# Kernel optimization log

Hardware: AMD Instinct MI355X
Metric: run time of the kernel (lower is better)

Reference implementation:

```python
import jax, jax.numpy as jnp
import numpy as np

N = 30000      # nodes
E = 300000     # edges (before self-loops)
F_NODE = 32; F_EDGE = 16
HID = 64       # hidden_channels
H = 4; C = 64  # heads, per-head channels (GATConv out_channels = HID)
NEG_SLOPE_ATT = 0.2   # GATConv negative_slope
NEG_SLOPE_ACT = 0.01  # F.leaky_relu default
LN_EPS = 1e-5


def setup_inputs() -> dict:
    key = jax.random.key(0)
    ks = jax.random.split(key, 32)
    def w(k, shape, fan_in):
        return jax.random.normal(k, shape, jnp.float32) * (1.0 / np.sqrt(fan_in))
    inp = {
        "x": jax.random.normal(ks[0], (N, F_NODE), jnp.float32),
        "edge_index": jax.random.randint(ks[1], (2, E), 0, N),
        "edge_attr": jax.random.normal(ks[2], (E, F_EDGE), jnp.float32),
        "wn": w(ks[3], (F_NODE, HID), F_NODE), "bn": jnp.zeros((HID,), jnp.float32),
        "we": w(ks[4], (F_EDGE, HID), F_EDGE), "be": jnp.zeros((HID,), jnp.float32),
    }
    for i, off in ((1, 5), (2, 13)):
        inp[f"lin{i}"] = w(ks[off], (HID, H * C), HID)        # GATConv.lin
        inp[f"line{i}"] = w(ks[off + 1], (HID, H * C), HID)    # GATConv.lin_edge
        inp[f"as{i}"] = w(ks[off + 2], (H, C), C)              # att_src
        inp[f"ad{i}"] = w(ks[off + 3], (H, C), C)              # att_dst
        inp[f"ae{i}"] = w(ks[off + 4], (H, C), C)              # att_edge
        inp[f"b{i}"] = jnp.zeros((C,), jnp.float32)            # GATConv bias (concat=False -> C)
        inp[f"g{i}"] = jnp.ones((HID,), jnp.float32)           # LayerNorm weight
        inp[f"bt{i}"] = jnp.zeros((HID,), jnp.float32)         # LayerNorm bias
    return inp


def layernorm(x, g, b):
    mu = x.mean(-1, keepdims=True)
    v = ((x - mu) ** 2).mean(-1, keepdims=True)
    return (x - mu) / jnp.sqrt(v + LN_EPS) * g + b


def gat_layer(x, src, dst, e_attr, lin_w, lin_e_w, att_src, att_dst, att_edge, bias, n):
    # x: [n, HID]; e_attr: [E2, HID]; edge lists already include self-loops
    E2 = src.shape[0]
    h = (x @ lin_w).reshape(n, H, C)          # [n,H,C]
    e = (e_attr @ lin_e_w).reshape(E2, H, C)  # [E2,H,C]
    a_src = (h * att_src[None]).sum(-1)       # [n,H]
    a_dst = (h * att_dst[None]).sum(-1)       # [n,H]
    a_edge = (e * att_edge[None]).sum(-1)     # [E2,H]
    a = jax.nn.leaky_relu(a_src[src] + a_dst[dst] + a_edge, NEG_SLOPE_ATT)
    # scatter-softmax over destination neighborhoods (every node has a self-loop)
    m = jax.ops.segment_max(a, dst, num_segments=n)
    ex = jnp.exp(a - m[dst])
    den = jax.ops.segment_sum(ex, dst, num_segments=n)
    alpha = ex / den[dst]                     # [E2,H]
    out = jax.ops.segment_sum(h[src] * alpha[..., None], dst, num_segments=n)  # [n,H,C]
    return out.mean(axis=1) + bias, alpha     # concat=False: average heads


def reference(x, edge_index, edge_attr, wn, bn, we, be,
              lin1, line1, as1, ad1, ae1, b1, g1, bt1,
              lin2, line2, as2, ad2, ae2, b2, g2, bt2):
    n = x.shape[0]
    x = jax.nn.relu(x @ wn + bn)
    ea = jax.nn.relu(edge_attr @ we + be)
    src, dst = edge_index[0], edge_index[1]
    # PyG add_self_loops(fill_value='mean'): self-loop edge_attr = mean of incoming edge_attr
    ones = jnp.ones((src.shape[0],), ea.dtype)
    deg = jax.ops.segment_sum(ones, dst, num_segments=n)
    mean_ea = jax.ops.segment_sum(ea, dst, num_segments=n) / jnp.maximum(deg, 1.0)[:, None]
    loop = jnp.arange(n, dtype=src.dtype)
    src_f = jnp.concatenate([src, loop])
    dst_f = jnp.concatenate([dst, loop])
    ea_f = jnp.concatenate([ea, mean_ea], axis=0)
    h1, alpha1 = gat_layer(x, src_f, dst_f, ea_f, lin1, line1, as1, ad1, ae1, b1, n)
    h1 = layernorm(jax.nn.leaky_relu(h1, NEG_SLOPE_ACT), g1, bt1)
    # dropout is identity in eval mode
    h2, alpha2 = gat_layer(h1, src_f, dst_f, ea_f, lin2, line2, as2, ad2, ae2, b2, n)
    h2 = layernorm(jax.nn.leaky_relu(h2, NEG_SLOPE_ACT), g2, bt2)
    return h2, alpha1, alpha2
```

## Files before the change

kernel.cpp:

```cpp
#include <hip/hip_runtime.h>

#define FN 32
#define FE 16
#define HID 64
#define HEADS 4
#define CHC 64

typedef float f32x4 __attribute__((ext_vector_type(4)));

__device__ __forceinline__ float bf2f(unsigned short u) {
  unsigned int x = ((unsigned int)u) << 16;
  return __builtin_bit_cast(float, x);
}
__device__ __forceinline__ unsigned short f2bf(float f) {
  unsigned int x = __builtin_bit_cast(unsigned int, f);
  unsigned int r = (x + 0x7fff + ((x >> 16) & 1)) >> 16;
  return (unsigned short)r;
}
__device__ __forceinline__ unsigned int pack2bf(float a, float b) {
  return (unsigned int)f2bf(a) | ((unsigned int)f2bf(b) << 16);
}

__global__ __launch_bounds__(256) void k_vecs(
    const float* __restrict__ lin1, const float* __restrict__ line1,
    const float* __restrict__ as1, const float* __restrict__ ad1,
    const float* __restrict__ ae1,
    const float* __restrict__ lin2, const float* __restrict__ line2,
    const float* __restrict__ as2, const float* __restrict__ ad2,
    const float* __restrict__ ae2,
    float* __restrict__ vS, float* __restrict__ vD, float* __restrict__ vE)
{
  int bi = blockIdx.x;
  int l = bi / 3, kind = bi % 3;
  const float* lin = (kind == 2) ? (l ? line2 : line1) : (l ? lin2 : lin1);
  const float* att = (kind == 0) ? (l ? as2 : as1)
                   : (kind == 1) ? (l ? ad2 : ad1) : (l ? ae2 : ae1);
  float* out = ((kind == 0) ? vS : (kind == 1) ? vD : vE) + l * 256;
  int t = threadIdx.x;
  int c = t >> 2, hd = t & 3;
  float acc = 0.f;
  for (int cc = 0; cc < CHC; cc++)
    acc += lin[c * (HEADS * CHC) + hd * CHC + cc] * att[hd * CHC + cc];
  out[c * 4 + hd] = acc;
}

__global__ __launch_bounds__(256) void k_deg(const int* __restrict__ dst,
                                             int* __restrict__ deg, int E)
{
  int e = blockIdx.x * 256 + threadIdx.x;
  if (e < E) atomicAdd(&deg[dst[e]], 1);
}

__global__ __launch_bounds__(1024) void k_scan1(const int* __restrict__ deg,
    int* __restrict__ rowptr, int* __restrict__ bsum, int n)
{
  __shared__ int wsum[16];
  int t = threadIdx.x, wv = t >> 6, lane = t & 63;
  int i = blockIdx.x * 1024 + t;
  int val = (i < n) ? deg[i] : 0;
  int sc = val;
  #pragma unroll
  for (int off = 1; off < 64; off <<= 1) {
    int u = __shfl_up(sc, off);
    if (lane >= off) sc += u;
  }
  if (lane == 63) wsum[wv] = sc;
  __syncthreads();
  int woff = 0;
  #pragma unroll
  for (int k = 0; k < 16; k++) woff += (k < wv) ? wsum[k] : 0;
  if (i < n) rowptr[i] = woff + sc - val;
  if (t == 0) {
    int tot = 0;
    #pragma unroll
    for (int k = 0; k < 16; k++) tot += wsum[k];
    bsum[blockIdx.x] = tot;
  }
}

__global__ __launch_bounds__(1024) void k_scan23(const int* __restrict__ bsum,
    int* __restrict__ rowptr, int nb, int n)
{
  int b = blockIdx.x;
  int t = threadIdx.x;
  int off = 0;
  for (int j = 0; j < b; j++) off += bsum[j];
  int i = b * 1024 + t;
  if (i < n) rowptr[i] += off;
  if (b == 0 && t == 0) {
    int tot = 0;
    for (int j = 0; j < nb; j++) tot += bsum[j];
    rowptr[n] = tot;
  }
}

__global__ __launch_bounds__(256) void k_fill(const int* __restrict__ src,
    const int* __restrict__ dst, const int* __restrict__ rowptr,
    int* __restrict__ cnt, int* __restrict__ eid, int* __restrict__ srcs,
    int* __restrict__ perm, int E)
{
  int e = blockIdx.x * 256 + threadIdx.x;
  if (e < E) {
    int d = dst[e];
    int pos = rowptr[d] + atomicAdd(&cnt[d], 1);
    eid[pos] = e;
    srcs[pos] = src[e];
    perm[e] = pos;
  }
}

__global__ __launch_bounds__(256) void k_aeg_e(const float* __restrict__ eattr,
    const float* __restrict__ we, const float* __restrict__ be,
    const float* __restrict__ vE, const int* __restrict__ perm,
    float* __restrict__ aeg1, float* __restrict__ aeg2, int E)
{
  __shared__ float4 we_t4[HID][4];
  __shared__ float4 vE_s[2][HID];
  __shared__ float  be_s[HID];
  int t = threadIdx.x;
  for (int i = t; i < FE * HID; i += 256) {
    int k = i >> 6, c = i & 63;
    ((float*)we_t4)[c * 16 + k] = we[i];
  }
  for (int i = t; i < 512; i += 256) ((float*)vE_s)[i] = vE[i];
  if (t < HID) be_s[t] = be[t];
  __syncthreads();

  int e = blockIdx.x * 256 + t;
  if (e >= E) return;
  const float4* er = (const float4*)(eattr + (size_t)e * FE);
  float4 A = er[0], B = er[1], C4 = er[2], D = er[3];
  float ta[FE] = {A.x, A.y, A.z, A.w, B.x, B.y, B.z, B.w,
                  C4.x, C4.y, C4.z, C4.w, D.x, D.y, D.z, D.w};
  float4 acc1 = make_float4(0.f, 0.f, 0.f, 0.f);
  float4 acc2 = make_float4(0.f, 0.f, 0.f, 0.f);
  #pragma unroll 4
  for (int c = 0; c < HID; c++) {
    float4 w0 = we_t4[c][0], w1 = we_t4[c][1], w2 = we_t4[c][2], w3 = we_t4[c][3];
    float ea = be_s[c];
    ea += ta[0] * w0.x + ta[1] * w0.y + ta[2] * w0.z + ta[3] * w0.w;
    ea += ta[4] * w1.x + ta[5] * w1.y + ta[6] * w1.z + ta[7] * w1.w;
    ea += ta[8] * w2.x + ta[9] * w2.y + ta[10] * w2.z + ta[11] * w2.w;
    ea += ta[12] * w3.x + ta[13] * w3.y + ta[14] * w3.z + ta[15] * w3.w;
    ea = fmaxf(ea, 0.f);
    float4 u1 = vE_s[0][c], u2 = vE_s[1][c];
    acc1.x += ea * u1.x; acc1.y += ea * u1.y; acc1.z += ea * u1.z; acc1.w += ea * u1.w;
    acc2.x += ea * u2.x; acc2.y += ea * u2.y; acc2.z += ea * u2.z; acc2.w += ea * u2.w;
  }
  int pos = perm[e];
  *(float4*)(aeg1 + (size_t)pos * 4) = acc1;
  *(float4*)(aeg2 + (size_t)pos * 4) = acc2;
}

__global__ __launch_bounds__(256) void k_self_aeg(const int* __restrict__ rowptr,
    float* __restrict__ aeg1, float* __restrict__ aeg2, int E, int n)
{
  int t = threadIdx.x;
  int v = blockIdx.x * 32 + (t >> 3);
  if (v >= n) return;
  int ent = t & 7;
  int h = ent & 3;
  const float* srcp = (ent < 4) ? aeg1 : aeg2;
  int r0 = rowptr[v], r1 = rowptr[v + 1];
  float s = 0.f;
  for (int j = r0; j < r1; j++) s += srcp[(size_t)j * 4 + h];
  float m = s / fmaxf((float)(r1 - r0), 1.f);
  if (ent < 4) aeg1[((size_t)E + v) * 4 + h] = m;
  else         aeg2[((size_t)E + v) * 4 + h] = m;
}

__global__ __launch_bounds__(256) void k_hx1(const float* __restrict__ x,
    const float* __restrict__ wn, const float* __restrict__ bn,
    const float* __restrict__ vS, const float* __restrict__ vD,
    const float* __restrict__ lin, unsigned short* __restrict__ h_bf,
    float* __restrict__ ssrc, float* __restrict__ sdst, int n)
{
  int t = threadIdx.x, wv = t >> 6, lane = t & 63;
  int v0 = blockIdx.x * 16;
  __shared__ float xin_s[16][FN];
  __shared__ float xs[16][HID];
  if (t < 128) {
    int node = t >> 3, c4 = (t & 7) * 4;
    int vv = v0 + node;
    float4 val = make_float4(0.f, 0.f, 0.f, 0.f);
    if (vv < n) val = *(const float4*)(x + (size_t)vv * FN + c4);
    *(float4*)&xin_s[node][c4] = val;
  }
  __syncthreads();
  {
    int nd = t >> 4, cg = t & 15;
    int vv = v0 + nd;
    const float4* wn4 = (const float4*)wn;
    float4 a = ((const float4*)bn)[cg];
    #pragma unroll 8
    for (int k = 0; k < FN; k++) {
      float xv = xin_s[nd][k];
      float4 w = wn4[k * 16 + cg];
      a.x += xv * w.x; a.y += xv * w.y; a.z += xv * w.z; a.w += xv * w.w;
    }
    a.x = fmaxf(a.x, 0.f); a.y = fmaxf(a.y, 0.f);
    a.z = fmaxf(a.z, 0.f); a.w = fmaxf(a.w, 0.f);
    *(float4*)&xs[nd][cg * 4] = a;
    const float4* vS4 = (const float4*)vS;
    const float4* vD4 = (const float4*)vD;
    int c0 = cg * 4;
    float4 vs0 = vS4[c0], vs1 = vS4[c0 + 1], vs2 = vS4[c0 + 2], vs3 = vS4[c0 + 3];
    float4 vd0 = vD4[c0], vd1 = vD4[c0 + 1], vd2 = vD4[c0 + 2], vd3 = vD4[c0 + 3];
    float pS[4], pD[4];
    pS[0] = a.x * vs0.x + a.y * vs1.x + a.z * vs2.x + a.w * vs3.x;
    pS[1] = a.x * vs0.y + a.y * vs1.y + a.z * vs2.y + a.w * vs3.y;
    pS[2] = a.x * vs0.z + a.y * vs1.z + a.z * vs2.z + a.w * vs3.z;
    pS[3] = a.x * vs0.w + a.y * vs1.w + a.z * vs2.w + a.w * vs3.w;
    pD[0] = a.x * vd0.x + a.y * vd1.x + a.z * vd2.x + a.w * vd3.x;
    pD[1] = a.x * vd0.y + a.y * vd1.y + a.z * vd2.y + a.w * vd3.y;
    pD[2] = a.x * vd0.z + a.y * vd1.z + a.z * vd2.z + a.w * vd3.z;
    pD[3] = a.x * vd0.w + a.y * vd1.w + a.z * vd2.w + a.w * vd3.w;
    #pragma unroll
    for (int off = 1; off < 16; off <<= 1) {
      #pragma unroll
      for (int h = 0; h < 4; h++) {
        pS[h] += __shfl_xor(pS[h], off);
        pD[h] += __shfl_xor(pD[h], off);
      }
    }
    if (cg == 0 && vv < n) {
      *(float4*)(ssrc + (size_t)vv * 4) = make_float4(pS[0], pS[1], pS[2], pS[3]);
      *(float4*)(sdst + (size_t)vv * 4) = make_float4(pD[0], pD[1], pD[2], pD[3]);
    }
  }
  __syncthreads();
  float acc[4][4];
  #pragma unroll
  for (int i = 0; i < 4; i++)
    #pragma unroll
    for (int j = 0; j < 4; j++) acc[i][j] = 0.f;
  const float4* lin4 = (const float4*)lin;
  int nd0 = wv * 4;
  #pragma unroll 4
  for (int kb = 0; kb < 16; kb++) {
    float4 xv[4];
    #pragma unroll
    for (int i = 0; i < 4; i++) xv[i] = *(const float4*)&xs[nd0 + i][kb * 4];
    float4 lv0 = lin4[(kb * 4 + 0) * 64 + lane];
    float4 lv1 = lin4[(kb * 4 + 1) * 64 + lane];
    float4 lv2 = lin4[(kb * 4 + 2) * 64 + lane];
    float4 lv3 = lin4[(kb * 4 + 3) * 64 + lane];
    #pragma unroll
    for (int i = 0; i < 4; i++) {
      acc[i][0] += xv[i].x * lv0.x + xv[i].y * lv1.x + xv[i].z * lv2.x + xv[i].w * lv3.x;
      acc[i][1] += xv[i].x * lv0.y + xv[i].y * lv1.y + xv[i].z * lv2.y + xv[i].w * lv3.y;
      acc[i][2] += xv[i].x * lv0.z + xv[i].y * lv1.z + xv[i].z * lv2.z + xv[i].w * lv3.z;
      acc[i][3] += xv[i].x * lv0.w + xv[i].y * lv1.w + xv[i].z * lv2.w + xv[i].w * lv3.w;
    }
  }
  #pragma unroll
  for (int i = 0; i < 4; i++) {
    int v = v0 + nd0 + i;
    if (v < n) {
      uint2 u;
      u.x = pack2bf(acc[i][0], acc[i][1]);
      u.y = pack2bf(acc[i][2], acc[i][3]);
      *(uint2*)(h_bf + (size_t)v * 256 + lane * 4) = u;
    }
  }
}

__global__ __launch_bounds__(256) void k_h(const float* __restrict__ xin,
    const float* __restrict__ lin, unsigned short* __restrict__ h_bf, int n)
{
  int t = threadIdx.x, wv = t >> 6, lane = t & 63;
  int v0 = blockIdx.x * 16;
  __shared__ float xs[16][HID];
  {
    int node = t >> 4, ch4 = (t & 15) * 4;
    int vv = v0 + node;
    float4 val = make_float4(0.f, 0.f, 0.f, 0.f);
    if (vv < n) val = *(const float4*)(xin + (size_t)vv * HID + ch4);
    *(float4*)&xs[node][ch4] = val;
  }
  __syncthreads();
  float acc[4][4];
  #pragma unroll
  for (int i = 0; i < 4; i++)
    #pragma unroll
    for (int j = 0; j < 4; j++) acc[i][j] = 0.f;
  const float4* lin4 = (const float4*)lin;
  int nd0 = wv * 4;
  #pragma unroll 4
  for (int kb = 0; kb < 16; kb++) {
    float4 xv[4];
    #pragma unroll
    for (int i = 0; i < 4; i++) xv[i] = *(const float4*)&xs[nd0 + i][kb * 4];
    float4 lv0 = lin4[(kb * 4 + 0) * 64 + lane];
    float4 lv1 = lin4[(kb * 4 + 1) * 64 + lane];
    float4 lv2 = lin4[(kb * 4 + 2) * 64 + lane];
    float4 lv3 = lin4[(kb * 4 + 3) * 64 + lane];
    #pragma unroll
    for (int i = 0; i < 4; i++) {
      acc[i][0] += xv[i].x * lv0.x + xv[i].y * lv1.x + xv[i].z * lv2.x + xv[i].w * lv3.x;
      acc[i][1] += xv[i].x * lv0.y + xv[i].y * lv1.y + xv[i].z * lv2.y + xv[i].w * lv3.y;
      acc[i][2] += xv[i].x * lv0.z + xv[i].y * lv1.z + xv[i].z * lv2.z + xv[i].w * lv3.z;
      acc[i][3] += xv[i].x * lv0.w + xv[i].y * lv1.w + xv[i].z * lv2.w + xv[i].w * lv3.w;
    }
  }
  #pragma unroll
  for (int i = 0; i < 4; i++) {
    int v = v0 + nd0 + i;
    if (v < n) {
      uint2 u;
      u.x = pack2bf(acc[i][0], acc[i][1]);
      u.y = pack2bf(acc[i][2], acc[i][3]);
      *(uint2*)(h_bf + (size_t)v * 256 + lane * 4) = u;
    }
  }
}

template<bool DOTS>
__global__ __launch_bounds__(256) void k_node(
    const unsigned short* __restrict__ h_bf, const float* __restrict__ ssrc,
    const float* __restrict__ sdst, const float* __restrict__ aegc,
    const int* __restrict__ rowptr, const int* __restrict__ eidArr,
    const int* __restrict__ srcs, const float* __restrict__ bias,
    const float* __restrict__ gamma, const float* __restrict__ beta,
    const float* __restrict__ vS2, const float* __restrict__ vD2,
    float* __restrict__ alpha_out, float* __restrict__ xout,
    float* __restrict__ ssrc_o, float* __restrict__ sdst_o, int n, int E)
{
  __shared__ float als[4][4][72];
  __shared__ int   svec[4][72];
  int t = threadIdx.x; int wv = t >> 6, lane = t & 63;
  int v = blockIdx.x * 4 + wv;
  if (v >= n) return;
  int r0 = rowptr[v], r1 = rowptr[v + 1];
  int deg = r1 - r0, ne = deg + 1;
  int coff = lane * 4;
  int hh = lane >> 4;
  float acc0 = 0.f, acc1 = 0.f, acc2 = 0.f, acc3 = 0.f;
  const float4* aeg4 = (const float4*)aegc;
  const float4* ss4p = (const float4*)ssrc;
  float4 sd4 = ((const float4*)sdst)[v];

  if (ne <= 64) {
    int s = v, eo = E + v;
    if (lane < deg) { s = srcs[r0 + lane]; eo = eidArr[r0 + lane]; }
    bool valid = (lane < ne);
    float4 ae4 = aeg4[(lane < deg) ? (r0 + lane) : (E + v)];
    float4 ss4 = ss4p[s];
    svec[wv][lane] = s;
    if (lane < 8) svec[wv][64 + lane] = v;
    __builtin_amdgcn_wave_barrier();
    __builtin_amdgcn_sched_barrier(0);
    uint2 pu[16];
    {
      const int* svp = svec[wv];
      int4 sa = *(const int4*)(svp + 0);
      int4 sb = *(const int4*)(svp + 4);
      int4 sc_ = *(const int4*)(svp + 8);
      int4 se_ = *(const int4*)(svp + 12);
      pu[0]  = *(const uint2*)(h_bf + (size_t)sa.x * 256 + coff);
      pu[1]  = *(const uint2*)(h_bf + (size_t)sa.y * 256 + coff);
      pu[2]  = *(const uint2*)(h_bf + (size_t)sa.z * 256 + coff);
      pu[3]  = *(const uint2*)(h_bf + (size_t)sa.w * 256 + coff);
      pu[4]  = *(const uint2*)(h_bf + (size_t)sb.x * 256 + coff);
      pu[5]  = *(const uint2*)(h_bf + (size_t)sb.y * 256 + coff);
      pu[6]  = *(const uint2*)(h_bf + (size_t)sb.z * 256 + coff);
      pu[7]  = *(const uint2*)(h_bf + (size_t)sb.w * 256 + coff);
      pu[8]  = *(const uint2*)(h_bf + (size_t)sc_.x * 256 + coff);
      pu[9]  = *(const uint2*)(h_bf + (size_t)sc_.y * 256 + coff);
      pu[10] = *(const uint2*)(h_bf + (size_t)sc_.z * 256 + coff);
      pu[11] = *(const uint2*)(h_bf + (size_t)sc_.w * 256 + coff);
      pu[12] = *(const uint2*)(h_bf + (size_t)se_.x * 256 + coff);
      pu[13] = *(const uint2*)(h_bf + (size_t)se_.y * 256 + coff);
      pu[14] = *(const uint2*)(h_bf + (size_t)se_.z * 256 + coff);
      pu[15] = *(const uint2*)(h_bf + (size_t)se_.w * 256 + coff);
    }
    float a0 = -INFINITY, a1 = -INFINITY, a2 = -INFINITY, a3 = -INFINITY;
    if (valid) {
      a0 = ss4.x + sd4.x + ae4.x; a0 = (a0 > 0.f) ? a0 : 0.2f * a0;
      a1 = ss4.y + sd4.y + ae4.y; a1 = (a1 > 0.f) ? a1 : 0.2f * a1;
      a2 = ss4.z + sd4.z + ae4.z; a2 = (a2 > 0.f) ? a2 : 0.2f * a2;
      a3 = ss4.w + sd4.w + ae4.w; a3 = (a3 > 0.f) ? a3 : 0.2f * a3;
    }
    float m0, m1, m2, m3;
    {
      bool hi0 = lane & 1;
      float k0 = hi0 ? a2 : a0, s0 = hi0 ? a0 : a2;
      float k1 = hi0 ? a3 : a1, s1 = hi0 ? a1 : a3;
      float q0 = fmaxf(k0, __shfl_xor(s0, 1));
      float q1 = fmaxf(k1, __shfl_xor(s1, 1));
      bool hi1 = lane & 2;
      float k2 = hi1 ? q1 : q0, s2 = hi1 ? q0 : q1;
      float r = fmaxf(k2, __shfl_xor(s2, 2));
      r = fmaxf(r, __shfl_xor(r, 4));
      r = fmaxf(r, __shfl_xor(r, 8));
      r = fmaxf(r, __shfl_xor(r, 16));
      r = fmaxf(r, __shfl_xor(r, 32));
      m0 = __shfl(r, 0); m1 = __shfl(r, 2); m2 = __shfl(r, 1); m3 = __shfl(r, 3);
    }
    float e0 = __expf(a0 - m0), e1 = __expf(a1 - m1);
    float e2 = __expf(a2 - m2), e3 = __expf(a3 - m3);
    float d0, d1, d2, d3;
    {
      bool hi0 = lane & 1;
      float k0 = hi0 ? e2 : e0, s0 = hi0 ? e0 : e2;
      float k1 = hi0 ? e3 : e1, s1 = hi0 ? e1 : e3;
      float q0 = k0 + __shfl_xor(s0, 1);
      float q1 = k1 + __shfl_xor(s1, 1);
      bool hi1 = lane & 2;
      float k2 = hi1 ? q1 : q0, s2 = hi1 ? q0 : q1;
      float r = k2 + __shfl_xor(s2, 2);
      r += __shfl_xor(r, 4);
      r += __shfl_xor(r, 8);
      r += __shfl_xor(r, 16);
      r += __shfl_xor(r, 32);
      d0 = __shfl(r, 0); d1 = __shfl(r, 2); d2 = __shfl(r, 1); d3 = __shfl(r, 3);
    }
    float4 alf = make_float4(e0 / d0, e1 / d1, e2 / d2, e3 / d3);
    if (valid) {
      f32x4 alv = {alf.x, alf.y, alf.z, alf.w};
      __builtin_nontemporal_store(alv, (f32x4*)alpha_out + eo);
    }
    als[wv][0][lane] = alf.x;
    als[wv][1][lane] = alf.y;
    als[wv][2][lane] = alf.z;
    als[wv][3][lane] = alf.w;
    if (lane < 8) {
      als[wv][0][64 + lane] = 0.f;
      als[wv][1][64 + lane] = 0.f;
      als[wv][2][64 + lane] = 0.f;
      als[wv][3][64 + lane] = 0.f;
    }
    __builtin_amdgcn_wave_barrier();
    __builtin_amdgcn_sched_barrier(0);
    const float* alsh = als[wv][hh];
    {
      float4 al0 = *(const float4*)(alsh + 0);
      float4 al1 = *(const float4*)(alsh + 4);
      float4 al2 = *(const float4*)(alsh + 8);
      float4 al3 = *(const float4*)(alsh + 12);
      float alr[16] = {al0.x, al0.y, al0.z, al0.w, al1.x, al1.y, al1.z, al1.w,
                       al2.x, al2.y, al2.z, al2.w, al3.x, al3.y, al3.z, al3.w};
      #pragma unroll
      for (int j = 0; j < 16; j++) {
        float al = alr[j];
        acc0 += al * bf2f((unsigned short)(pu[j].x & 0xffff));
        acc1 += al * bf2f((unsigned short)(pu[j].x >> 16));
        acc2 += al * bf2f((unsigned short)(pu[j].y & 0xffff));
        acc3 += al * bf2f((unsigned short)(pu[j].y >> 16));
      }
    }
    const int* svp = svec[wv];
    for (int jj = 16; jj < ne; jj += 8) {
      int4 sv0 = *(const int4*)(svp + jj);
      int4 sv1 = *(const int4*)(svp + jj + 4);
      float4 al0 = *(const float4*)(alsh + jj);
      float4 al1 = *(const float4*)(alsh + jj + 4);
      uint2 u0 = *(const uint2*)(h_bf + (size_t)sv0.x * 256 + coff);
      uint2 u1 = *(const uint2*)(h_bf + (size_t)sv0.y * 256 + coff);
      uint2 u2 = *(const uint2*)(h_bf + (size_t)sv0.z * 256 + coff);
      uint2 u3 = *(const uint2*)(h_bf + (size_t)sv0.w * 256 + coff);
      uint2 u4 = *(const uint2*)(h_bf + (size_t)sv1.x * 256 + coff);
      uint2 u5 = *(const uint2*)(h_bf + (size_t)sv1.y * 256 + coff);
      uint2 u6 = *(const uint2*)(h_bf + (size_t)sv1.z * 256 + coff);
      uint2 u7 = *(const uint2*)(h_bf + (size_t)sv1.w * 256 + coff);
      acc0 += al0.x * bf2f((unsigned short)(u0.x & 0xffff))
            + al0.y * bf2f((unsigned short)(u1.x & 0xffff))
            + al0.z * bf2f((unsigned short)(u2.x & 0xffff))
            + al0.w * bf2f((unsigned short)(u3.x & 0xffff))
            + al1.x * bf2f((unsigned short)(u4.x & 0xffff))
            + al1.y * bf2f((unsigned short)(u5.x & 0xffff))
            + al1.z * bf2f((unsigned short)(u6.x & 0xffff))
            + al1.w * bf2f((unsigned short)(u7.x & 0xffff));
      acc1 += al0.x * bf2f((unsigned short)(u0.x >> 16))
            + al0.y * bf2f((unsigned short)(u1.x >> 16))
            + al0.z * bf2f((unsigned short)(u2.x >> 16))
            + al0.w * bf2f((unsigned short)(u3.x >> 16))
            + al1.x * bf2f((unsigned short)(u4.x >> 16))
            + al1.y * bf2f((unsigned short)(u5.x >> 16))
            + al1.z * bf2f((unsigned short)(u6.x >> 16))
            + al1.w * bf2f((unsigned short)(u7.x >> 16));
      acc2 += al0.x * bf2f((unsigned short)(u0.y & 0xffff))
            + al0.y * bf2f((unsigned short)(u1.y & 0xffff))
            + al0.z * bf2f((unsigned short)(u2.y & 0xffff))
            + al0.w * bf2f((unsigned short)(u3.y & 0xffff))
            + al1.x * bf2f((unsigned short)(u4.y & 0xffff))
            + al1.y * bf2f((unsigned short)(u5.y & 0xffff))
            + al1.z * bf2f((unsigned short)(u6.y & 0xffff))
            + al1.w * bf2f((unsigned short)(u7.y & 0xffff));
      acc3 += al0.x * bf2f((unsigned short)(u0.y >> 16))
            + al0.y * bf2f((unsigned short)(u1.y >> 16))
            + al0.z * bf2f((unsigned short)(u2.y >> 16))
            + al0.w * bf2f((unsigned short)(u3.y >> 16))
            + al1.x * bf2f((unsigned short)(u4.y >> 16))
            + al1.y * bf2f((unsigned short)(u5.y >> 16))
            + al1.z * bf2f((unsigned short)(u6.y >> 16))
            + al1.w * bf2f((unsigned short)(u7.y >> 16));
    }
  } else {
    int j4 = lane >> 2, hb = lane & 3;
    float sd = sdst[v * 4 + hb];
    float m = -INFINITY;
    for (int jb = 0; jb < ne; jb += 16) {
      int jc = jb + j4;
      if (jc < ne) {
        int s2 = (jc < deg) ? srcs[r0 + jc] : v;
        float ae = (jc < deg) ? aegc[(size_t)(r0 + jc) * 4 + hb]
                              : aegc[((size_t)E + v) * 4 + hb];
        float a = ssrc[s2 * 4 + hb] + sd + ae;
        a = (a > 0.f) ? a : 0.2f * a;
        m = fmaxf(m, a);
      }
    }
    m = fmaxf(m, __shfl_xor(m, 4));
    m = fmaxf(m, __shfl_xor(m, 8));
    m = fmaxf(m, __shfl_xor(m, 16));
    m = fmaxf(m, __shfl_xor(m, 32));
    float den = 0.f;
    for (int jb = 0; jb < ne; jb += 16) {
      int jc = jb + j4;
      if (jc < ne) {
        int s2 = (jc < deg) ? srcs[r0 + jc] : v;
        float ae = (jc < deg) ? aegc[(size_t)(r0 + jc) * 4 + hb]
                              : aegc[((size_t)E + v) * 4 + hb];
        float a = ssrc[s2 * 4 + hb] + sd + ae;
        a = (a > 0.f) ? a : 0.2f * a;
        den += __expf(a - m);
      }
    }
    den += __shfl_xor(den, 4);
    den += __shfl_xor(den, 8);
    den += __shfl_xor(den, 16);
    den += __shfl_xor(den, 32);
    float rden = 1.f / den;
    for (int jb = 0; jb < ne; jb += 16) {
      int jc = jb + j4;
      if (jc < ne) {
        int s2 = (jc < deg) ? srcs[r0 + jc] : v;
        int eo = (jc < deg) ? eidArr[r0 + jc] : E + v;
        float ae = (jc < deg) ? aegc[(size_t)(r0 + jc) * 4 + hb]
                              : aegc[((size_t)E + v) * 4 + hb];
        float a = ssrc[s2 * 4 + hb] + sd + ae;
        a = (a > 0.f) ? a : 0.2f * a;
        alpha_out[(size_t)eo * 4 + hb] = __expf(a - m) * rden;
      }
    }
    float sdh = __shfl(sd, hh);
    float mh  = __shfl(m, hh);
    float rdh = __shfl(rden, hh);
    for (int jc = 0; jc < ne; jc++) {
      int s0 = (jc < deg) ? srcs[r0 + jc] : v;
      size_t ap = (jc < deg) ? (size_t)(r0 + jc) : (size_t)E + v;
      float a = ssrc[s0 * 4 + hh] + sdh + aegc[ap * 4 + hh];
      a = (a > 0.f) ? a : 0.2f * a;
      float al = __expf(a - mh) * rdh;
      uint2 u = *(const uint2*)(h_bf + (size_t)s0 * 256 + coff);
      acc0 += al * bf2f((unsigned short)(u.x & 0xffff));
      acc1 += al * bf2f((unsigned short)(u.x >> 16));
      acc2 += al * bf2f((unsigned short)(u.y & 0xffff));
      acc3 += al * bf2f((unsigned short)(u.y >> 16));
    }
  }

  acc0 += __shfl_xor(acc0, 16); acc0 += __shfl_xor(acc0, 32);
  acc1 += __shfl_xor(acc1, 16); acc1 += __shfl_xor(acc1, 32);
  acc2 += __shfl_xor(acc2, 16); acc2 += __shfl_xor(acc2, 32);
  acc3 += __shfl_xor(acc3, 16); acc3 += __shfl_xor(acc3, 32);

  int c16 = lane & 15;
  float4 b4 = ((const float4*)bias)[c16];
  float v0 = acc0 * 0.25f + b4.x;
  float v1 = acc1 * 0.25f + b4.y;
  float v2 = acc2 * 0.25f + b4.z;
  float v3 = acc3 * 0.25f + b4.w;
  v0 = (v0 > 0.f) ? v0 : 0.01f * v0;
  v1 = (v1 > 0.f) ? v1 : 0.01f * v1;
  v2 = (v2 > 0.f) ? v2 : 0.01f * v2;
  v3 = (v3 > 0.f) ? v3 : 0.01f * v3;
  float mu = v0 + v1 + v2 + v3;
  mu += __shfl_xor(mu, 1); mu += __shfl_xor(mu, 2);
  mu += __shfl_xor(mu, 4); mu += __shfl_xor(mu, 8);
  mu *= (1.f / 64.f);
  float d0 = v0 - mu, d1 = v1 - mu, d2 = v2 - mu, d3 = v3 - mu;
  float var = d0 * d0 + d1 * d1 + d2 * d2 + d3 * d3;
  var += __shfl_xor(var, 1); var += __shfl_xor(var, 2);
  var += __shfl_xor(var, 4); var += __shfl_xor(var, 8);
  var *= (1.f / 64.f);
  float rstd = rsqrtf(var + 1e-5f);
  float4 g4 = ((const float4*)gamma)[c16];
  float4 be4 = ((const float4*)beta)[c16];
  float y0 = d0 * rstd * g4.x + be4.x;
  float y1 = d1 * rstd * g4.y + be4.y;
  float y2 = d2 * rstd * g4.z + be4.z;
  float y3 = d3 * rstd * g4.w + be4.w;
  if (lane < 16) {
    float4 y = make_float4(y0, y1, y2, y3);
    *(float4*)(xout + (size_t)v * HID + lane * 4) = y;
  }
  if constexpr (DOTS) {
    int c0 = c16 * 4;
    float4 vs0 = ((const float4*)vS2)[c0],     vs1 = ((const float4*)vS2)[c0 + 1];
    float4 vs2 = ((const float4*)vS2)[c0 + 2], vs3 = ((const float4*)vS2)[c0 + 3];
    float4 vd0 = ((const float4*)vD2)[c0],     vd1 = ((const float4*)vD2)[c0 + 1];
    float4 vd2 = ((const float4*)vD2)[c0 + 2], vd3 = ((const float4*)vD2)[c0 + 3];
    float pS[4], pD[4];
    pS[0] = y0 * vs0.x + y1 * vs1.x + y2 * vs2.x + y3 * vs3.x;
    pS[1] = y0 * vs0.y + y1 * vs1.y + y2 * vs2.y + y3 * vs3.y;
    pS[2] = y0 * vs0.z + y1 * vs1.z + y2 * vs2.z + y3 * vs3.z;
    pS[3] = y0 * vs0.w + y1 * vs1.w + y2 * vs2.w + y3 * vs3.w;
    pD[0] = y0 * vd0.x + y1 * vd1.x + y2 * vd2.x + y3 * vd3.x;
    pD[1] = y0 * vd0.y + y1 * vd1.y + y2 * vd2.y + y3 * vd3.y;
    pD[2] = y0 * vd0.z + y1 * vd1.z + y2 * vd2.z + y3 * vd3.z;
    pD[3] = y0 * vd0.w + y1 * vd1.w + y2 * vd2.w + y3 * vd3.w;
    #pragma unroll
    for (int off = 1; off < 16; off <<= 1) {
      #pragma unroll
      for (int h = 0; h < 4; h++) {
        pS[h] += __shfl_xor(pS[h], off);
        pD[h] += __shfl_xor(pD[h], off);
      }
    }
    if (lane == 0) {
      *(float4*)(ssrc_o + (size_t)v * 4) = make_float4(pS[0], pS[1], pS[2], pS[3]);
      *(float4*)(sdst_o + (size_t)v * 4) = make_float4(pD[0], pD[1], pD[2], pD[3]);
    }
  }
}

extern "C" void kernel_launch(void* const* d_in, const int* in_sizes, int n_in,
                              void* d_out, int out_size, void* d_ws, size_t ws_size,
                              hipStream_t stream)
{
  const float* x     = (const float*)d_in[0];
  const int*   eidx  = (const int*)d_in[1];
  const float* eattr = (const float*)d_in[2];
  const float* wn    = (const float*)d_in[3];
  const float* bn    = (const float*)d_in[4];
  const float* we    = (const float*)d_in[5];
  const float* be    = (const float*)d_in[6];
  const float* lin1  = (const float*)d_in[7];
  const float* line1 = (const float*)d_in[8];
  const float* as1   = (const float*)d_in[9];
  const float* ad1   = (const float*)d_in[10];
  const float* ae1   = (const float*)d_in[11];
  const float* b1    = (const float*)d_in[12];
  const float* g1    = (const float*)d_in[13];
  const float* bt1   = (const float*)d_in[14];
  const float* lin2  = (const float*)d_in[15];
  const float* line2 = (const float*)d_in[16];
  const float* as2   = (const float*)d_in[17];
  const float* ad2   = (const float*)d_in[18];
  const float* ae2   = (const float*)d_in[19];
  const float* b2    = (const float*)d_in[20];
  const float* g2    = (const float*)d_in[21];
  const float* bt2   = (const float*)d_in[22];

  int n = in_sizes[0] / FN;
  int E = in_sizes[1] / 2;
  const int* srcA = eidx;
  const int* dstA = eidx + E;

  float* out_h2 = (float*)d_out;
  float* alpha1 = out_h2 + (size_t)n * HID;
  float* alpha2 = alpha1 + (size_t)(E + n) * 4;

  char* ws = (char*)d_ws;
  size_t off = 0;
  auto alloc = [&](size_t bytes) -> char* {
    char* p = ws + off;
    off += (bytes + 255) & ~(size_t)255;
    return p;
  };
  unsigned short* h_bf = (unsigned short*)alloc((size_t)n * 256 * 2);
  float* h1      = (float*)alloc((size_t)n * HID * 4);
  float* aeg1c   = (float*)alloc((size_t)(E + n) * 4 * 4);
  float* aeg2c   = (float*)alloc((size_t)(E + n) * 4 * 4);
  float* ssrc1   = (float*)alloc((size_t)n * 4 * 4);
  float* sdst1   = (float*)alloc((size_t)n * 4 * 4);
  float* ssrc2   = (float*)alloc((size_t)n * 4 * 4);
  float* sdst2   = (float*)alloc((size_t)n * 4 * 4);
  float* vS      = (float*)alloc(512 * 4);
  float* vD      = (float*)alloc(512 * 4);
  float* vE      = (float*)alloc(512 * 4);
  int*   deg     = (int*)alloc((size_t)n * 4);
  int*   cnt     = (int*)alloc((size_t)n * 4);
  int*   rowptr  = (int*)alloc((size_t)(n + 1) * 4);
  int*   eid     = (int*)alloc((size_t)E * 4);
  int*   srcs    = (int*)alloc((size_t)E * 4);
  int*   perm    = (int*)alloc((size_t)E * 4);
  int*   bsum    = (int*)alloc(1024 * 4);

  hipMemsetAsync(deg, 0, (size_t)n * 4, stream);
  hipMemsetAsync(cnt, 0, (size_t)n * 4, stream);

  int nb = (n + 1023) / 1024;
  k_vecs<<<6, 256, 0, stream>>>(lin1, line1, as1, ad1, ae1,
                                lin2, line2, as2, ad2, ae2, vS, vD, vE);
  k_deg<<<(E + 255) / 256, 256, 0, stream>>>(dstA, deg, E);
  k_scan1<<<nb, 1024, 0, stream>>>(deg, rowptr, bsum, n);
  k_scan23<<<nb, 1024, 0, stream>>>(bsum, rowptr, nb, n);
  k_fill<<<(E + 255) / 256, 256, 0, stream>>>(srcA, dstA, rowptr, cnt, eid, srcs, perm, E);
  k_aeg_e<<<(E + 255) / 256, 256, 0, stream>>>(eattr, we, be, vE, perm, aeg1c, aeg2c, E);
  k_self_aeg<<<(n + 31) / 32, 256, 0, stream>>>(rowptr, aeg1c, aeg2c, E, n);

  k_hx1<<<(n + 15) / 16, 256, 0, stream>>>(x, wn, bn, vS, vD, lin1, h_bf,
                                           ssrc1, sdst1, n);
  k_node<true><<<(n + 3) / 4, 256, 0, stream>>>(h_bf, ssrc1, sdst1, aeg1c,
      rowptr, eid, srcs, b1, g1, bt1, vS + 256, vD + 256,
      alpha1, h1, ssrc2, sdst2, n, E);
  k_h<<<(n + 15) / 16, 256, 0, stream>>>(h1, lin2, h_bf, n);
  k_node<false><<<(n + 3) / 4, 256, 0, stream>>>(h_bf, ssrc2, sdst2, aeg2c,
      rowptr, eid, srcs, b2, g2, bt2, nullptr, nullptr,
      alpha2, out_h2, nullptr, nullptr, n, E);
}
```

Baseline: 226.9 us.

## Fuse graph preprocessing into one cooperative kernel and simplify node gather loop

```diff
diff --git a/kernel.cpp b/kernel.cpp
--- a/kernel.cpp
+++ b/kernel.cpp
@@ -1,4 +1,7 @@
 #include <hip/hip_runtime.h>
+#include <hip/hip_cooperative_groups.h>
+
+namespace cg = cooperative_groups;
 
 #define FN 32
 #define FE 16
@@ -21,103 +24,90 @@
   return (unsigned int)f2bf(a) | ((unsigned int)f2bf(b) << 16);
 }
 
-__global__ __launch_bounds__(256) void k_vecs(
+__global__ __launch_bounds__(256) void k_prep(
+    const int* __restrict__ eidx, const float* __restrict__ eattr,
+    const float* __restrict__ we, const float* __restrict__ be,
     const float* __restrict__ lin1, const float* __restrict__ line1,
     const float* __restrict__ as1, const float* __restrict__ ad1,
     const float* __restrict__ ae1,
     const float* __restrict__ lin2, const float* __restrict__ line2,
     const float* __restrict__ as2, const float* __restrict__ ad2,
     const float* __restrict__ ae2,
-    float* __restrict__ vS, float* __restrict__ vD, float* __restrict__ vE)
+    float* __restrict__ vS, float* __restrict__ vD, float* __restrict__ vE,
+    int* __restrict__ deg, int* __restrict__ cnt, int* __restrict__ rowptr,
+    int* __restrict__ bsum, int* __restrict__ eid, int* __restrict__ srcs,
+    float* __restrict__ aeg1, float* __restrict__ aeg2, int n, int E)
 {
-  int bi = blockIdx.x;
-  int l = bi / 3, kind = bi % 3;
-  const float* lin = (kind == 2) ? (l ? line2 : line1) : (l ? lin2 : lin1);
-  const float* att = (kind == 0) ? (l ? as2 : as1)
-                   : (kind == 1) ? (l ? ad2 : ad1) : (l ? ae2 : ae1);
-  float* out = ((kind == 0) ? vS : (kind == 1) ? vD : vE) + l * 256;
-  int t = threadIdx.x;
-  int c = t >> 2, hd = t & 3;
-  float acc = 0.f;
-  for (int cc = 0; cc < CHC; cc++)
-    acc += lin[c * (HEADS * CHC) + hd * CHC + cc] * att[hd * CHC + cc];
-  out[c * 4 + hd] = acc;
-}
-
-__global__ __launch_bounds__(256) void k_deg(const int* __restrict__ dst,
-                                             int* __restrict__ deg, int E)
-{
-  int e = blockIdx.x * 256 + threadIdx.x;
-  if (e < E) atomicAdd(&deg[dst[e]], 1);
-}
-
-__global__ __launch_bounds__(1024) void k_scan1(const int* __restrict__ deg,
-    int* __restrict__ rowptr, int* __restrict__ bsum, int n)
-{
-  __shared__ int wsum[16];
-  int t = threadIdx.x, wv = t >> 6, lane = t & 63;
-  int i = blockIdx.x * 1024 + t;
-  int val = (i < n) ? deg[i] : 0;
-  int sc = val;
-  #pragma unroll
-  for (int off = 1; off < 64; off <<= 1) {
-    int u = __shfl_up(sc, off);
-    if (lane >= off) sc += u;
-  }
-  if (lane == 63) wsum[wv] = sc;
-  __syncthreads();
-  int woff = 0;
-  #pragma unroll
-  for (int k = 0; k < 16; k++) woff += (k < wv) ? wsum[k] : 0;
-  if (i < n) rowptr[i] = woff + sc - val;
-  if (t == 0) {
-    int tot = 0;
-    #pragma unroll
-    for (int k = 0; k < 16; k++) tot += wsum[k];
-    bsum[blockIdx.x] = tot;
-  }
-}
-
-__global__ __launch_bounds__(1024) void k_scan23(const int* __restrict__ bsum,
-    int* __restrict__ rowptr, int nb, int n)
-{
-  int b = blockIdx.x;
-  int t = threadIdx.x;
-  int off = 0;
-  for (int j = 0; j < b; j++) off += bsum[j];
-  int i = b * 1024 + t;
-  if (i < n) rowptr[i] += off;
+  cg::grid_group grid = cg::this_grid();
+  int t = threadIdx.x, b = blockIdx.x;
+  int gsz = gridDim.x * 256;
+  int gtid = b * 256 + t;
+  const int* srcA = eidx;
+  const int* dstA = eidx + E;
+
+  for (int i = gtid; i < n; i += gsz) deg[i] = 0;
+  if (b < 6) {
+    int l = b / 3, kind = b % 3;
+    const float* lin = (kind == 2) ? (l ? line2 : line1) : (l ? lin2 : lin1);
+    const float* att = (kind == 0) ? (l ? as2 : as1)
+                     : (kind == 1) ? (l ? ad2 : ad1) : (l ? ae2 : ae1);
+    float* out = ((kind == 0) ? vS : (kind == 1) ? vD : vE) + l * 256;
+    int c = t >> 2, hd = t & 3;
+    float acc = 0.f;
+    for (int cc = 0; cc < CHC; cc++)
+      acc += lin[c * (HEADS * CHC) + hd * CHC + cc] * att[hd * CHC + cc];
+    out[c * 4 + hd] = acc;
+  }
+  grid.sync();
+
+  for (int e = gtid; e < E; e += gsz) atomicAdd(&deg[dstA[e]], 1);
+  grid.sync();
+
+  int nbs = (n + 255) / 256;
+  __shared__ int wsum[4];
+  if (b < nbs) {
+    int lane = t & 63, wv = t >> 6;
+    int i = b * 256 + t;
+    int val = (i < n) ? deg[i] : 0;
+    int sc = val;
+    #pragma unroll
+    for (int off = 1; off < 64; off <<= 1) {
+      int u = __shfl_up(sc, off);
+      if (lane >= off) sc += u;
+    }
+    if (lane == 63) wsum[wv] = sc;
+    __syncthreads();
+    int woff = 0;
+    #pragma unroll
+    for (int k = 0; k < 4; k++) woff += (k < wv) ? wsum[k] : 0;
+    if (i < n) rowptr[i] = woff + sc - val;
+    if (t == 0) {
+      int tot = wsum[0] + wsum[1] + wsum[2] + wsum[3];
+      bsum[b] = tot;
+    }
+  }
+  grid.sync();
+
+  if (b < nbs) {
+    int off = 0;
+    for (int j = 0; j < b; j++) off += bsum[j];
+    int i = b * 256 + t;
+    if (i < n) {
+      int rv = rowptr[i] + off;
+      rowptr[i] = rv;
+      cnt[i] = rv;
+    }
+  }
   if (b == 0 && t == 0) {
     int tot = 0;
-    for (int j = 0; j < nb; j++) tot += bsum[j];
+    for (int j = 0; j < nbs; j++) tot += bsum[j];
     rowptr[n] = tot;
   }
-}
-
-__global__ __launch_bounds__(256) void k_fill(const int* __restrict__ src,
-    const int* __restrict__ dst, const int* __restrict__ rowptr,
-    int* __restrict__ cnt, int* __restrict__ eid, int* __restrict__ srcs,
-    int* __restrict__ perm, int E)
-{
-  int e = blockIdx.x * 256 + threadIdx.x;
-  if (e < E) {
-    int d = dst[e];
-    int pos = rowptr[d] + atomicAdd(&cnt[d], 1);
-    eid[pos] = e;
-    srcs[pos] = src[e];
-    perm[e] = pos;
-  }
-}
-
-__global__ __launch_bounds__(256) void k_aeg_e(const float* __restrict__ eattr,
-    const float* __restrict__ we, const float* __restrict__ be,
-    const float* __restrict__ vE, const int* __restrict__ perm,
-    float* __restrict__ aeg1, float* __restrict__ aeg2, int E)
-{
+  grid.sync();
+
   __shared__ float4 we_t4[HID][4];
   __shared__ float4 vE_s[2][HID];
   __shared__ float  be_s[HID];
-  int t = threadIdx.x;
   for (int i = t; i < FE * HID; i += 256) {
     int k = i >> 6, c = i & 63;
     ((float*)we_t4)[c * 16 + k] = we[i];
@@ -125,48 +115,46 @@
   for (int i = t; i < 512; i += 256) ((float*)vE_s)[i] = vE[i];
   if (t < HID) be_s[t] = be[t];
   __syncthreads();
-
-  int e = blockIdx.x * 256 + t;
-  if (e >= E) return;
-  const float4* er = (const float4*)(eattr + (size_t)e * FE);
-  float4 A = er[0], B = er[1], C4 = er[2], D = er[3];
-  float ta[FE] = {A.x, A.y, A.z, A.w, B.x, B.y, B.z, B.w,
-                  C4.x, C4.y, C4.z, C4.w, D.x, D.y, D.z, D.w};
-  float4 acc1 = make_float4(0.f, 0.f, 0.f, 0.f);
-  float4 acc2 = make_float4(0.f, 0.f, 0.f, 0.f);
-  #pragma unroll 4
-  for (int c = 0; c < HID; c++) {
-    float4 w0 = we_t4[c][0], w1 = we_t4[c][1], w2 = we_t4[c][2], w3 = we_t4[c][3];
-    float ea = be_s[c];
-    ea += ta[0] * w0.x + ta[1] * w0.y + ta[2] * w0.z + ta[3] * w0.w;
-    ea += ta[4] * w1.x + ta[5] * w1.y + ta[6] * w1.z + ta[7] * w1.w;
-    ea += ta[8] * w2.x + ta[9] * w2.y + ta[10] * w2.z + ta[11] * w2.w;
-    ea += ta[12] * w3.x + ta[13] * w3.y + ta[14] * w3.z + ta[15] * w3.w;
-    ea = fmaxf(ea, 0.f);
-    float4 u1 = vE_s[0][c], u2 = vE_s[1][c];
-    acc1.x += ea * u1.x; acc1.y += ea * u1.y; acc1.z += ea * u1.z; acc1.w += ea * u1.w;
-    acc2.x += ea * u2.x; acc2.y += ea * u2.y; acc2.z += ea * u2.z; acc2.w += ea * u2.w;
-  }
-  int pos = perm[e];
-  *(float4*)(aeg1 + (size_t)pos * 4) = acc1;
-  *(float4*)(aeg2 + (size_t)pos * 4) = acc2;
-}
-
-__global__ __launch_bounds__(256) void k_self_aeg(const int* __restrict__ rowptr,
-    float* __restrict__ aeg1, float* __restrict__ aeg2, int E, int n)
-{
-  int t = threadIdx.x;
-  int v = blockIdx.x * 32 + (t >> 3);
-  if (v >= n) return;
-  int ent = t & 7;
-  int h = ent & 3;
-  const float* srcp = (ent < 4) ? aeg1 : aeg2;
-  int r0 = rowptr[v], r1 = rowptr[v + 1];
-  float s = 0.f;
-  for (int j = r0; j < r1; j++) s += srcp[(size_t)j * 4 + h];
-  float m = s / fmaxf((float)(r1 - r0), 1.f);
-  if (ent < 4) aeg1[((size_t)E + v) * 4 + h] = m;
-  else         aeg2[((size_t)E + v) * 4 + h] = m;
+  for (int e = gtid; e < E; e += gsz) {
+    int d = dstA[e];
+    int pos = atomicAdd(&cnt[d], 1);
+    eid[pos] = e;
+    srcs[pos] = srcA[e];
+    const float4* er = (const float4*)(eattr + (size_t)e * FE);
+    float4 A = er[0], B = er[1], C4 = er[2], D = er[3];
+    float ta[FE] = {A.x, A.y, A.z, A.w, B.x, B.y, B.z, B.w,
+                    C4.x, C4.y, C4.z, C4.w, D.x, D.y, D.z, D.w};
+    float4 acc1 = make_float4(0.f, 0.f, 0.f, 0.f);
+    float4 acc2 = make_float4(0.f, 0.f, 0.f, 0.f);
+    #pragma unroll 4
+    for (int c = 0; c < HID; c++) {
+      float4 w0 = we_t4[c][0], w1 = we_t4[c][1], w2 = we_t4[c][2], w3 = we_t4[c][3];
+      float ea = be_s[c];
+      ea += ta[0] * w0.x + ta[1] * w0.y + ta[2] * w0.z + ta[3] * w0.w;
+      ea += ta[4] * w1.x + ta[5] * w1.y + ta[6] * w1.z + ta[7] * w1.w;
+      ea += ta[8] * w2.x + ta[9] * w2.y + ta[10] * w2.z + ta[11] * w2.w;
+      ea += ta[12] * w3.x + ta[13] * w3.y + ta[14] * w3.z + ta[15] * w3.w;
+      ea = fmaxf(ea, 0.f);
+      float4 u1 = vE_s[0][c], u2 = vE_s[1][c];
+      acc1.x += ea * u1.x; acc1.y += ea * u1.y; acc1.z += ea * u1.z; acc1.w += ea * u1.w;
+      acc2.x += ea * u2.x; acc2.y += ea * u2.y; acc2.z += ea * u2.z; acc2.w += ea * u2.w;
+    }
+    *(float4*)(aeg1 + (size_t)pos * 4) = acc1;
+    *(float4*)(aeg2 + (size_t)pos * 4) = acc2;
+  }
+  grid.sync();
+
+  for (int w = gtid; w < n * 8; w += gsz) {
+    int v = w >> 3;
+    int ent = w & 7, h = ent & 3;
+    const float* sp = (ent < 4) ? aeg1 : aeg2;
+    int r0 = rowptr[v], r1 = rowptr[v + 1];
+    float s = 0.f;
+    for (int j = r0; j < r1; j++) s += sp[(size_t)j * 4 + h];
+    float m = s / fmaxf((float)(r1 - r0), 1.f);
+    if (ent < 4) aeg1[((size_t)E + v) * 4 + h] = m;
+    else         aeg2[((size_t)E + v) * 4 + h] = m;
+  }
 }
 
 __global__ __launch_bounds__(256) void k_hx1(const float* __restrict__ x,
@@ -188,22 +176,22 @@
   }
   __syncthreads();
   {
-    int nd = t >> 4, cg = t & 15;
+    int nd = t >> 4, cg_ = t & 15;
     int vv = v0 + nd;
     const float4* wn4 = (const float4*)wn;
-    float4 a = ((const float4*)bn)[cg];
+    float4 a = ((const float4*)bn)[cg_];
     #pragma unroll 8
     for (int k = 0; k < FN; k++) {
       float xv = xin_s[nd][k];
-      float4 w = wn4[k * 16 + cg];
+      float4 w = wn4[k * 16 + cg_];
       a.x += xv * w.x; a.y += xv * w.y; a.z += xv * w.z; a.w += xv * w.w;
     }
     a.x = fmaxf(a.x, 0.f); a.y = fmaxf(a.y, 0.f);
     a.z = fmaxf(a.z, 0.f); a.w = fmaxf(a.w, 0.f);
-    *(float4*)&xs[nd][cg * 4] = a;
+    *(float4*)&xs[nd][cg_ * 4] = a;
     const float4* vS4 = (const float4*)vS;
     const float4* vD4 = (const float4*)vD;
-    int c0 = cg * 4;
+    int c0 = cg_ * 4;
     float4 vs0 = vS4[c0], vs1 = vS4[c0 + 1], vs2 = vS4[c0 + 2], vs3 = vS4[c0 + 3];
     float4 vd0 = vD4[c0], vd1 = vD4[c0 + 1], vd2 = vD4[c0 + 2], vd3 = vD4[c0 + 3];
     float pS[4], pD[4];
@@ -223,7 +211,7 @@
         pD[h] += __shfl_xor(pD[h], off);
       }
     }
-    if (cg == 0 && vv < n) {
+    if (cg_ == 0 && vv < n) {
       *(float4*)(ssrc + (size_t)vv * 4) = make_float4(pS[0], pS[1], pS[2], pS[3]);
       *(float4*)(sdst + (size_t)vv * 4) = make_float4(pD[0], pD[1], pD[2], pD[3]);
     }
@@ -326,8 +314,7 @@
     float* __restrict__ alpha_out, float* __restrict__ xout,
     float* __restrict__ ssrc_o, float* __restrict__ sdst_o, int n, int E)
 {
-  __shared__ float als[4][4][72];
-  __shared__ int   svec[4][72];
+  __shared__ float als[4][64][4];
   int t = threadIdx.x; int wv = t >> 6, lane = t & 63;
   int v = blockIdx.x * 4 + wv;
   if (v >= n) return;
@@ -344,38 +331,10 @@
     int s = v, eo = E + v;
     if (lane < deg) { s = srcs[r0 + lane]; eo = eidArr[r0 + lane]; }
     bool valid = (lane < ne);
-    float4 ae4 = aeg4[(lane < deg) ? (r0 + lane) : (E + v)];
-    float4 ss4 = ss4p[s];
-    svec[wv][lane] = s;
-    if (lane < 8) svec[wv][64 + lane] = v;
-    __builtin_amdgcn_wave_barrier();
-    __builtin_amdgcn_sched_barrier(0);
-    uint2 pu[16];
-    {
-      const int* svp = svec[wv];
-      int4 sa = *(const int4*)(svp + 0);
-      int4 sb = *(const int4*)(svp + 4);
-      int4 sc_ = *(const int4*)(svp + 8);
-      int4 se_ = *(const int4*)(svp + 12);
-      pu[0]  = *(const uint2*)(h_bf + (size_t)sa.x * 256 + coff);
-      pu[1]  = *(const uint2*)(h_bf + (size_t)sa.y * 256 + coff);
-      pu[2]  = *(const uint2*)(h_bf + (size_t)sa.z * 256 + coff);
-      pu[3]  = *(const uint2*)(h_bf + (size_t)sa.w * 256 + coff);
-      pu[4]  = *(const uint2*)(h_bf + (size_t)sb.x * 256 + coff);
-      pu[5]  = *(const uint2*)(h_bf + (size_t)sb.y * 256 + coff);
-      pu[6]  = *(const uint2*)(h_bf + (size_t)sb.z * 256 + coff);
-      pu[7]  = *(const uint2*)(h_bf + (size_t)sb.w * 256 + coff);
-      pu[8]  = *(const uint2*)(h_bf + (size_t)sc_.x * 256 + coff);
-      pu[9]  = *(const uint2*)(h_bf + (size_t)sc_.y * 256 + coff);
-      pu[10] = *(const uint2*)(h_bf + (size_t)sc_.z * 256 + coff);
-      pu[11] = *(const uint2*)(h_bf + (size_t)sc_.w * 256 + coff);
-      pu[12] = *(const uint2*)(h_bf + (size_t)se_.x * 256 + coff);
-      pu[13] = *(const uint2*)(h_bf + (size_t)se_.y * 256 + coff);
-      pu[14] = *(const uint2*)(h_bf + (size_t)se_.z * 256 + coff);
-      pu[15] = *(const uint2*)(h_bf + (size_t)se_.w * 256 + coff);
-    }
     float a0 = -INFINITY, a1 = -INFINITY, a2 = -INFINITY, a3 = -INFINITY;
     if (valid) {
+      float4 ae4 = aeg4[(lane < deg) ? (r0 + lane) : (E + v)];
+      float4 ss4 = ss4p[s];
       a0 = ss4.x + sd4.x + ae4.x; a0 = (a0 > 0.f) ? a0 : 0.2f * a0;
       a1 = ss4.y + sd4.y + ae4.y; a1 = (a1 > 0.f) ? a1 : 0.2f * a1;
       a2 = ss4.z + sd4.z + ae4.z; a2 = (a2 > 0.f) ? a2 : 0.2f * a2;
@@ -420,81 +379,44 @@
       f32x4 alv = {alf.x, alf.y, alf.z, alf.w};
       __builtin_nontemporal_store(alv, (f32x4*)alpha_out + eo);
     }
-    als[wv][0][lane] = alf.x;
-    als[wv][1][lane] = alf.y;
-    als[wv][2][lane] = alf.z;
-    als[wv][3][lane] = alf.w;
-    if (lane < 8) {
-      als[wv][0][64 + lane] = 0.f;
-      als[wv][1][64 + lane] = 0.f;
-      als[wv][2][64 + lane] = 0.f;
-      als[wv][3][64 + lane] = 0.f;
-    }
+    *(float4*)als[wv][lane] = alf;
     __builtin_amdgcn_wave_barrier();
     __builtin_amdgcn_sched_barrier(0);
-    const float* alsh = als[wv][hh];
-    {
-      float4 al0 = *(const float4*)(alsh + 0);
-      float4 al1 = *(const float4*)(alsh + 4);
-      float4 al2 = *(const float4*)(alsh + 8);
-      float4 al3 = *(const float4*)(alsh + 12);
-      float alr[16] = {al0.x, al0.y, al0.z, al0.w, al1.x, al1.y, al1.z, al1.w,
-                       al2.x, al2.y, al2.z, al2.w, al3.x, al3.y, al3.z, al3.w};
-      #pragma unroll
-      for (int j = 0; j < 16; j++) {
-        float al = alr[j];
-        acc0 += al * bf2f((unsigned short)(pu[j].x & 0xffff));
-        acc1 += al * bf2f((unsigned short)(pu[j].x >> 16));
-        acc2 += al * bf2f((unsigned short)(pu[j].y & 0xffff));
-        acc3 += al * bf2f((unsigned short)(pu[j].y >> 16));
-      }
-    }
-    const int* svp = svec[wv];
-    for (int jj = 16; jj < ne; jj += 8) {
-      int4 sv0 = *(const int4*)(svp + jj);
-      int4 sv1 = *(const int4*)(svp + jj + 4);
-      float4 al0 = *(const float4*)(alsh + jj);
-      float4 al1 = *(const float4*)(alsh + jj + 4);
-      uint2 u0 = *(const uint2*)(h_bf + (size_t)sv0.x * 256 + coff);
-      uint2 u1 = *(const uint2*)(h_bf + (size_t)sv0.y * 256 + coff);
-      uint2 u2 = *(const uint2*)(h_bf + (size_t)sv0.z * 256 + coff);
-      uint2 u3 = *(const uint2*)(h_bf + (size_t)sv0.w * 256 + coff);
-      uint2 u4 = *(const uint2*)(h_bf + (size_t)sv1.x * 256 + coff);
-      uint2 u5 = *(const uint2*)(h_bf + (size_t)sv1.y * 256 + coff);
-      uint2 u6 = *(const uint2*)(h_bf + (size_t)sv1.z * 256 + coff);
-      uint2 u7 = *(const uint2*)(h_bf + (size_t)sv1.w * 256 + coff);
-      acc0 += al0.x * bf2f((unsigned short)(u0.x & 0xffff))
-            + al0.y * bf2f((unsigned short)(u1.x & 0xffff))
-            + al0.z * bf2f((unsigned short)(u2.x & 0xffff))
-            + al0.w * bf2f((unsigned short)(u3.x & 0xffff))
-            + al1.x * bf2f((unsigned short)(u4.x & 0xffff))
-            + al1.y * bf2f((unsigned short)(u5.x & 0xffff))
-            + al1.z * bf2f((unsigned short)(u6.x & 0xffff))
-            + al1.w * bf2f((unsigned short)(u7.x & 0xffff));
-      acc1 += al0.x * bf2f((unsigned short)(u0.x >> 16))
-            + al0.y * bf2f((unsigned short)(u1.x >> 16))
-            + al0.z * bf2f((unsigned short)(u2.x >> 16))
-            + al0.w * bf2f((unsigned short)(u3.x >> 16))
-            + al1.x * bf2f((unsigned short)(u4.x >> 16))
-            + al1.y * bf2f((unsigned short)(u5.x >> 16))
-            + al1.z * bf2f((unsigned short)(u6.x >> 16))
-            + al1.w * bf2f((unsigned short)(u7.x >> 16));
-      acc2 += al0.x * bf2f((unsigned short)(u0.y & 0xffff))
-            + al0.y * bf2f((unsigned short)(u1.y & 0xffff))
-            + al0.z * bf2f((unsigned short)(u2.y & 0xffff))
-            + al0.w * bf2f((unsigned short)(u3.y & 0xffff))
-            + al1.x * bf2f((unsigned short)(u4.y & 0xffff))
-            + al1.y * bf2f((unsigned short)(u5.y & 0xffff))
-            + al1.z * bf2f((unsigned short)(u6.y & 0xffff))
-            + al1.w * bf2f((unsigned short)(u7.y & 0xffff));
-      acc3 += al0.x * bf2f((unsigned short)(u0.y >> 16))
-            + al0.y * bf2f((unsigned short)(u1.y >> 16))
-            + al0.z * bf2f((unsigned short)(u2.y >> 16))
-            + al0.w * bf2f((unsigned short)(u3.y >> 16))
-            + al1.x * bf2f((unsigned short)(u4.y >> 16))
-            + al1.y * bf2f((unsigned short)(u5.y >> 16))
-            + al1.z * bf2f((unsigned short)(u6.y >> 16))
-            + al1.w * bf2f((unsigned short)(u7.y >> 16));
+    int jj = 0;
+    for (; jj + 3 < ne; jj += 4) {
+      int s0 = __shfl(s, jj), s1 = __shfl(s, jj + 1);
+      int s2 = __shfl(s, jj + 2), s3 = __shfl(s, jj + 3);
+      float al0 = als[wv][jj][hh],     al1 = als[wv][jj + 1][hh];
+      float al2 = als[wv][jj + 2][hh], al3 = als[wv][jj + 3][hh];
+      uint2 u0 = *(const uint2*)(h_bf + (size_t)s0 * 256 + coff);
+      uint2 u1 = *(const uint2*)(h_bf + (size_t)s1 * 256 + coff);
+      uint2 u2 = *(const uint2*)(h_bf + (size_t)s2 * 256 + coff);
+      uint2 u3 = *(const uint2*)(h_bf + (size_t)s3 * 256 + coff);
+      acc0 += al0 * bf2f((unsigned short)(u0.x & 0xffff))
+            + al1 * bf2f((unsigned short)(u1.x & 0xffff))
+            + al2 * bf2f((unsigned short)(u2.x & 0xffff))
+            + al3 * bf2f((unsigned short)(u3.x & 0xffff));
+      acc1 += al0 * bf2f((unsigned short)(u0.x >> 16))
+            + al1 * bf2f((unsigned short)(u1.x >> 16))
+            + al2 * bf2f((unsigned short)(u2.x >> 16))
+            + al3 * bf2f((unsigned short)(u3.x >> 16));
+      acc2 += al0 * bf2f((unsigned short)(u0.y & 0xffff))
+            + al1 * bf2f((unsigned short)(u1.y & 0xffff))
+            + al2 * bf2f((unsigned short)(u2.y & 0xffff))
+            + al3 * bf2f((unsigned short)(u3.y & 0xffff));
+      acc3 += al0 * bf2f((unsigned short)(u0.y >> 16))
+            + al1 * bf2f((unsigned short)(u1.y >> 16))
+            + al2 * bf2f((unsigned short)(u2.y >> 16))
+            + al3 * bf2f((unsigned short)(u3.y >> 16));
+    }
+    for (; jj < ne; jj++) {
+      int s0 = __shfl(s, jj);
+      float al0 = als[wv][jj][hh];
+      uint2 u0 = *(const uint2*)(h_bf + (size_t)s0 * 256 + coff);
+      acc0 += al0 * bf2f((unsigned short)(u0.x & 0xffff));
+      acc1 += al0 * bf2f((unsigned short)(u0.x >> 16));
+      acc2 += al0 * bf2f((unsigned short)(u0.y & 0xffff));
+      acc3 += al0 * bf2f((unsigned short)(u0.y >> 16));
     }
   } else {
     int j4 = lane >> 2, hb = lane & 3;
@@ -656,8 +578,6 @@
 
   int n = in_sizes[0] / FN;
   int E = in_sizes[1] / 2;
-  const int* srcA = eidx;
-  const int* dstA = eidx + E;
 
   float* out_h2 = (float*)d_out;
   float* alpha1 = out_h2 + (size_t)n * HID;
@@ -686,21 +606,18 @@
   int*   rowptr  = (int*)alloc((size_t)(n + 1) * 4);
   int*   eid     = (int*)alloc((size_t)E * 4);
   int*   srcs    = (int*)alloc((size_t)E * 4);
-  int*   perm    = (int*)alloc((size_t)E * 4);
   int*   bsum    = (int*)alloc(1024 * 4);
 
-  hipMemsetAsync(deg, 0, (size_t)n * 4, stream);
-  hipMemsetAsync(cnt, 0, (size_t)n * 4, stream);
-
-  int nb = (n + 1023) / 1024;
-  k_vecs<<<6, 256, 0, stream>>>(lin1, line1, as1, ad1, ae1,
-                                lin2, line2, as2, ad2, ae2, vS, vD, vE);
-  k_deg<<<(E + 255) / 256, 256, 0, stream>>>(dstA, deg, E);
-  k_scan1<<<nb, 1024, 0, stream>>>(deg, rowptr, bsum, n);
-  k_scan23<<<nb, 1024, 0, stream>>>(bsum, rowptr, nb, n);
-  k_fill<<<(E + 255) / 256, 256, 0, stream>>>(srcA, dstA, rowptr, cnt, eid, srcs, perm, E);
-  k_aeg_e<<<(E + 255) / 256, 256, 0, stream>>>(eattr, we, be, vE, perm, aeg1c, aeg2c, E);
-  k_self_aeg<<<(n + 31) / 32, 256, 0, stream>>>(rowptr, aeg1c, aeg2c, E, n);
+  void* args[] = {
+    (void*)&eidx, (void*)&eattr, (void*)&we, (void*)&be,
+    (void*)&lin1, (void*)&line1, (void*)&as1, (void*)&ad1, (void*)&ae1,
+    (void*)&lin2, (void*)&line2, (void*)&as2, (void*)&ad2, (void*)&ae2,
+    (void*)&vS, (void*)&vD, (void*)&vE,
+    (void*)&deg, (void*)&cnt, (void*)&rowptr, (void*)&bsum,
+    (void*)&eid, (void*)&srcs, (void*)&aeg1c, (void*)&aeg2c,
+    (void*)&n, (void*)&E
+  };
+  hipLaunchCooperativeKernel((void*)k_prep, dim3(512), dim3(256), args, 0, stream);
 
   k_hx1<<<(n + 15) / 16, 256, 0, stream>>>(x, wn, bn, vS, vD, lin1, h_bf,
                                            ssrc1, sdst1, n);
```

Measured after the change: 484.4 us. 2.13x slower.
